# Performance work log

Measured on AMD Instinct MI355X. Metric: run time of the kernel, lower is better.

Reference implementation:

```python
import jax, jax.numpy as jnp
import numpy as np

N, E, H, NH, RBF = 20000, 200000, 128, 8, 64
HD = H // NH
CUT_HI = 5.0


def _ln(t, s, b, eps=1e-6):
    mu = t.mean(-1, keepdims=True)
    var = ((t - mu) ** 2).mean(-1, keepdims=True)
    return (t - mu) * jax.lax.rsqrt(var + eps) * s + b


def _cutoff(w):
    # cosine cutoff, cutoff_lower = 0
    return 0.5 * (jnp.cos(w * (jnp.pi / CUT_HI)) + 1.0) * (w < CUT_HI)


def _xavier(k, fi, fo):
    lim = float(np.sqrt(6.0 / (fi + fo)))
    return jax.random.uniform(k, (fi, fo), minval=-lim, maxval=lim, dtype=jnp.float32)


def setup_inputs() -> dict:
    key = jax.random.key(0)
    ks = jax.random.split(key, 16)
    return {
        "x": jax.random.normal(ks[0], (N, H), jnp.float32),
        "vec": jax.random.normal(ks[1], (N, 3, H), jnp.float32),
        "edge_weight": jax.random.uniform(ks[2], (E, 1), jnp.float32) * 6.0,
        "edge_attr": jax.random.uniform(ks[3], (E, RBF), jnp.float32),
        "edge_vec": jax.random.normal(ks[4], (E, 3), jnp.float32),
        "senders": jax.random.randint(ks[5], (E,), 0, N, jnp.int32),
        "receivers": jax.random.randint(ks[6], (E,), 0, N, jnp.int32),
        "ln_s": jnp.ones((H,), jnp.float32), "ln_b": jnp.zeros((H,), jnp.float32),
        "Wq": _xavier(ks[7], H, H), "bq": jnp.zeros((H,), jnp.float32),
        "Wk": _xavier(ks[8], H, H), "bk": jnp.zeros((H,), jnp.float32),
        "Wv": _xavier(ks[9], H, 3 * H), "bv": jnp.zeros((3 * H,), jnp.float32),
        "Wvec": _xavier(ks[10], H, 3 * H),
        "Wdk": _xavier(ks[11], RBF, H), "bdk": jnp.zeros((H,), jnp.float32),
        "Wdv": _xavier(ks[12], RBF, 3 * H), "bdv": jnp.zeros((3 * H,), jnp.float32),
        "Wo": _xavier(ks[13], H, 3 * H), "bo": jnp.zeros((3 * H,), jnp.float32),
        "qln_s": jnp.ones((HD,), jnp.float32), "qln_b": jnp.zeros((HD,), jnp.float32),
        "kln_s": jnp.ones((HD,), jnp.float32), "kln_b": jnp.zeros((HD,), jnp.float32),
    }


def reference(x, vec, edge_weight, edge_attr, edge_vec, senders, receivers,
              ln_s, ln_b, Wq, bq, Wk, bk, Wv, bv, Wvec, Wdk, bdk, Wdv, bdv,
              Wo, bo, qln_s, qln_b, kln_s, kln_b):
    act = jax.nn.silu
    n = x.shape[0]
    xn = _ln(x, ln_s, ln_b)                                    # [N,H]
    q = _ln((xn @ Wq + bq).reshape(n, NH, HD), qln_s, qln_b)   # [N,h,d]
    k = _ln((xn @ Wk + bk).reshape(n, NH, HD), kln_s, kln_b)   # [N,h,d]
    v = (xn @ Wv + bv).reshape(n, NH, 3 * HD)                  # [N,h,3d]
    vp = vec @ Wvec                                            # [N,3,3H]
    vec1, vec2, vec3 = jnp.split(vp, 3, axis=-1)               # [N,3,H] each
    vec_dot = (vec1 * vec2).sum(axis=1)                        # [N,H]
    vec_h = vec.reshape(n, 3, NH, HD)                          # [N,3,h,d]
    dk = act(edge_attr @ Wdk + bdk).reshape(-1, NH, HD)        # [E,h,d]
    dv = act(edge_attr @ Wdv + bdv).reshape(-1, NH, 3 * HD)    # [E,h,3d]
    # message
    attn = (q[receivers] * k[senders] * dk).sum(axis=-1)       # [E,h]
    attn = act(attn) * _cutoff(edge_weight)                    # [E,h]
    v_j = v[senders] * dv                                      # [E,h,3d]
    xm, m1, m2 = jnp.split(v_j, 3, axis=2)                     # [E,h,d]
    xm = xm * attn[:, :, None]                                 # [E,h,d]
    vec_m = vec_h[senders] * m1[:, None] + m2[:, None] * edge_vec[:, :, None, None]  # [E,3,h,d]
    # aggregate
    x_agg = jax.ops.segment_sum(xm, receivers, num_segments=n).reshape(n, H)
    vec_agg = jax.ops.segment_sum(vec_m, receivers, num_segments=n).reshape(n, 3, H)
    o1, o2, o3 = jnp.split(x_agg @ Wo + bo, 3, axis=1)         # [N,H] each
    dvec = vec3 * o1[:, None] + vec_agg                        # [N,3,H]
    dx = vec_dot * o2 + o3                                     # [N,H]
    return (dx, dvec)
```

## Files before the change

kernel.cpp:

```cpp
#include <hip/hip_runtime.h>
#include <stdint.h>

#define NN 20000
#define NE 200000

typedef __attribute__((ext_vector_type(8))) short bf16x8;
typedef __attribute__((ext_vector_type(4))) float f32x4;

__device__ __forceinline__ float bf2f(uint32_t u) {
  union { uint32_t i; float f; } v; v.i = u << 16; return v.f;
}
__device__ __forceinline__ uint16_t f2bf(float f) {
  union { float f; uint32_t i; } v; v.f = f;
  return (uint16_t)((v.i + 0x7fffu + ((v.i >> 16) & 1u)) >> 16);
}
__device__ __forceinline__ uint32_t pk2(float lo, float hi) {
  return (uint32_t)f2bf(lo) | ((uint32_t)f2bf(hi) << 16);
}
__device__ __forceinline__ float siluf(float x) { return x / (1.f + __expf(-x)); }
__device__ __forceinline__ float prod2(uint32_t q2, uint32_t k2, uint32_t d2) {
  return bf2f(q2 & 0xffffu) * bf2f(k2 & 0xffffu) * bf2f(d2 & 0xffffu)
       + bf2f(q2 >> 16) * bf2f(k2 >> 16) * bf2f(d2 >> 16);
}

__global__ void k_prep(const float* __restrict__ Wq, const float* __restrict__ Wk,
                       const float* __restrict__ Wv, const float* __restrict__ Wvec,
                       const float* __restrict__ Wdk, const float* __restrict__ Wdv,
                       const float* __restrict__ Wo, const float* __restrict__ bq,
                       const float* __restrict__ bk, const float* __restrict__ bv,
                       const float* __restrict__ bdk, const float* __restrict__ bdv,
                       uint16_t* __restrict__ WTqkv, uint16_t* __restrict__ WTvec,
                       uint16_t* __restrict__ WTdkv2, uint16_t* __restrict__ WTo,
                       float* __restrict__ Bqkv, float* __restrict__ Bdkv2) {
  int idx = blockIdx.x * 256 + threadIdx.x;
  if (idx < 81920) {
    int j = idx;
    float v;
    if (j < 16384)      { int c = j >> 7, k = j & 127; v = Wq[k * 128 + c]; }
    else if (j < 32768) { j -= 16384; int c = j >> 7, k = j & 127; v = Wk[k * 128 + c]; }
    else                { j -= 32768; int c = j >> 7, k = j & 127; v = Wv[k * 384 + c]; }
    WTqkv[idx] = f2bf(v);
    return;
  }
  idx -= 81920;
  if (idx < 49152) {
    int c = idx >> 7, k = idx & 127;
    WTvec[idx] = f2bf(Wvec[k * 384 + c]);
    return;
  }
  idx -= 49152;
  if (idx < 32768) {
    int rr = idx >> 6, k = idx & 63;
    float v;
    if (rr < 128) v = Wdk[k * 128 + rr];
    else {
      int j = rr - 128, p = j >> 7, hd = j & 127;
      int c = (hd >> 4) * 48 + p * 16 + (hd & 15);
      v = Wdv[k * 384 + c];
    }
    WTdkv2[idx] = f2bf(v);
    return;
  }
  idx -= 32768;
  if (idx < 49152) {
    int c = idx >> 7, k = idx & 127;
    WTo[idx] = f2bf(Wo[k * 384 + c]);
    return;
  }
  idx -= 49152;
  if (idx < 640) Bqkv[idx] = (idx < 128) ? bq[idx] : ((idx < 256) ? bk[idx - 128] : bv[idx - 256]);
  else if (idx < 1152) {
    int t = idx - 640;
    if (t < 128) Bdkv2[t] = bdk[t];
    else {
      int j = t - 128, p = j >> 7, hd = j & 127;
      Bdkv2[t] = bdv[(hd >> 4) * 48 + p * 16 + (hd & 15)];
    }
  }
}

__global__ void k_node_pre(const float* __restrict__ x, const float* __restrict__ s,
                           const float* __restrict__ b, const float* __restrict__ vec,
                           uint16_t* __restrict__ xn_b, uint16_t* __restrict__ vec_b) {
  if (blockIdx.x < 5000) {
    int gt = blockIdx.x * 256 + threadIdx.x;
    int node = gt >> 6, lane = gt & 63;
    if (node >= NN) return;
    const float* row = x + (size_t)node * 128;
    float2 v = *(const float2*)&row[lane * 2];
    float sum = v.x + v.y, sq = v.x * v.x + v.y * v.y;
    #pragma unroll
    for (int off = 32; off; off >>= 1) { sum += __shfl_xor(sum, off); sq += __shfl_xor(sq, off); }
    float mu = sum * (1.f / 128.f);
    float var = sq * (1.f / 128.f) - mu * mu;
    float rs = rsqrtf(var + 1e-6f);
    float o0 = (v.x - mu) * rs * s[lane * 2] + b[lane * 2];
    float o1 = (v.y - mu) * rs * s[lane * 2 + 1] + b[lane * 2 + 1];
    ((uint32_t*)xn_b)[(size_t)node * 64 + lane] = pk2(o0, o1);
  } else {
    int i = (blockIdx.x - 5000) * 256 + threadIdx.x;
    if (i >= NN * 3 * 64) return;
    float2 v = ((const float2*)vec)[i];
    ((uint32_t*)vec_b)[i] = pk2(v.x, v.y);
  }
}

__global__ void k_cast_bf16(const float* __restrict__ src, uint16_t* __restrict__ dst, int npairs) {
  int i = blockIdx.x * 256 + threadIdx.x;
  if (i >= npairs) return;
  float2 v = ((const float2*)src)[i];
  ((uint32_t*)dst)[i] = pk2(v.x, v.y);
}

__global__ void k_hist(const int* __restrict__ rcv, int* __restrict__ deg) {
  int e = blockIdx.x * 256 + threadIdx.x;
  if (e < NE) atomicAdd(&deg[rcv[e]], 1);
}

__global__ void k_scan1(const int* __restrict__ deg, int* __restrict__ bsum) {
  __shared__ int ws[4];
  int i = blockIdx.x * 256 + threadIdx.x;
  int x = (i < NN) ? deg[i] : 0;
  #pragma unroll
  for (int d = 32; d; d >>= 1) x += __shfl_xor(x, d);
  if ((threadIdx.x & 63) == 0) ws[threadIdx.x >> 6] = x;
  __syncthreads();
  if (threadIdx.x == 0) bsum[blockIdx.x] = ws[0] + ws[1] + ws[2] + ws[3];
}

__global__ void k_scan2(int* __restrict__ bsum, int nb, int* __restrict__ off) {
  int lane = threadIdx.x;
  int carry = 0;
  for (int base = 0; base < nb; base += 64) {
    int i = base + lane;
    int x = (i < nb) ? bsum[i] : 0;
    int v = x;
    #pragma unroll
    for (int d = 1; d < 64; d <<= 1) { int y = __shfl_up(v, d); if (lane >= d) v += y; }
    if (i < nb) bsum[i] = carry + v - x;
    carry += __shfl(v, 63);
  }
  if (lane == 0) off[NN] = carry;
}

__global__ void k_scan3(const int* __restrict__ deg, const int* __restrict__ bsum,
                        int* __restrict__ off, int* __restrict__ cur) {
  __shared__ int ws[4];
  int t = threadIdx.x, lane = t & 63, w = t >> 6;
  int i = blockIdx.x * 256 + t;
  int x = (i < NN) ? deg[i] : 0;
  int v = x;
  #pragma unroll
  for (int d = 1; d < 64; d <<= 1) { int y = __shfl_up(v, d); if (lane >= d) v += y; }
  if (lane == 63) ws[w] = v;
  __syncthreads();
  int wadd = 0;
  for (int j = 0; j < w; j++) wadd += ws[j];
  int excl = bsum[blockIdx.x] + wadd + v - x;
  if (i < NN) { off[i] = excl; cur[i] = excl; }
}

__global__ void k_scatter(const int* __restrict__ rcv, int* __restrict__ cur,
                          int* __restrict__ perm) {
  int e = blockIdx.x * 256 + threadIdx.x;
  if (e >= NE) return;
  int pos = atomicAdd(&cur[rcv[e]], 1);
  perm[pos] = e;
}

__global__ void k_permute(const float* __restrict__ ea, const int* __restrict__ perm,
                          const int* __restrict__ snd, const int* __restrict__ rcv,
                          const float* __restrict__ ew, const float* __restrict__ evec,
                          uint16_t* __restrict__ ea_perm, int* __restrict__ sndp,
                          int* __restrict__ rcvp, float4* __restrict__ edata) {
  int idx = blockIdx.x * 256 + threadIdx.x;
  if (idx >= NE * 16) return;
  int i = idx >> 4, j = idx & 15;
  int e = perm[i];
  float4 v = *(const float4*)&ea[(size_t)e * 64 + j * 4];
  uint2 o;
  o.x = pk2(v.x, v.y);
  o.y = pk2(v.z, v.w);
  *(uint2*)&ea_perm[(size_t)i * 64 + j * 4] = o;
  if (j == 0) {
    sndp[i] = snd[e];
    rcvp[i] = rcv[e];
    float w = ew[e];
    float cut = (w < 5.f) ? 0.5f * (__cosf(w * 0.628318530717958648f) + 1.f) : 0.f;
    edata[i] = make_float4(evec[e * 3], evec[e * 3 + 1], evec[e * 3 + 2], cut);
  }
}

template <int KTOT, bool OUT_BF16, bool SILU>
__global__ __launch_bounds__(256) void k_gemm(const uint16_t* __restrict__ A,
                                              const uint16_t* __restrict__ BT,
                                              const float* __restrict__ bias,
                                              void* __restrict__ Cout, int M, int Fo) {
  __shared__ __align__(16) uint16_t As[128 * 72];
  __shared__ __align__(16) uint16_t Bs[128 * 72];
  int t = threadIdx.x;
  int l = t & 63;
  int row0 = blockIdx.y * 128, col0 = blockIdx.x * 128;
  int wm = ((t >> 6) >> 1) * 64, wn = ((t >> 6) & 1) * 64;
  f32x4 acc[4][4] = {};
  for (int kt = 0; kt < KTOT; kt += 64) {
    __syncthreads();
    #pragma unroll
    for (int i = 0; i < 4; i++) {
      int c = i * 256 + t;
      int row = c >> 3, ko = (c & 7) * 8;
      uint4 av = make_uint4(0u, 0u, 0u, 0u);
      int gr = row0 + row;
      if (gr < M) av = *(const uint4*)&A[(size_t)gr * KTOT + kt + ko];
      *(uint4*)&As[row * 72 + ko] = av;
      uint4 bw = *(const uint4*)&BT[(size_t)(col0 + row) * KTOT + kt + ko];
      *(uint4*)&Bs[row * 72 + ko] = bw;
    }
    __syncthreads();
    #pragma unroll
    for (int kk = 0; kk < 64; kk += 32) {
      bf16x8 af[4], bfr[4];
      #pragma unroll
      for (int mf = 0; mf < 4; mf++)
        af[mf] = *(const bf16x8*)&As[(wm + mf * 16 + (l & 15)) * 72 + (l >> 4) * 8 + kk];
      #pragma unroll
      for (int nf = 0; nf < 4; nf++)
        bfr[nf] = *(const bf16x8*)&Bs[(wn + nf * 16 + (l & 15)) * 72 + (l >> 4) * 8 + kk];
      #pragma unroll
      for (int mf = 0; mf < 4; mf++)
        #pragma unroll
        for (int nf = 0; nf < 4; nf++)
          acc[mf][nf] = __builtin_amdgcn_mfma_f32_16x16x32_bf16(af[mf], bfr[nf], acc[mf][nf], 0, 0, 0);
    }
  }
  float* Cf = (float*)Cout;
  uint16_t* Cb = (uint16_t*)Cout;
  #pragma unroll
  for (int mf = 0; mf < 4; mf++) {
    #pragma unroll
    for (int r = 0; r < 4; r++) {
      int grow = row0 + wm + mf * 16 + (l >> 4) * 4 + r;
      if (grow >= M) continue;
      #pragma unroll
      for (int nf = 0; nf < 4; nf++) {
        int gcol = col0 + wn + nf * 16 + (l & 15);
        float v = acc[mf][nf][r];
        if (bias) v += bias[gcol];
        if (SILU) v = siluf(v);
        if (OUT_BF16) Cb[(size_t)grow * Fo + gcol] = f2bf(v);
        else          Cf[(size_t)grow * Fo + gcol] = v;
      }
    }
  }
}

__global__ void k_headln(const uint16_t* __restrict__ qkv, const float* __restrict__ qs,
                         const float* __restrict__ qb, const float* __restrict__ ks,
                         const float* __restrict__ kb, uint16_t* __restrict__ out) {
  int idx = blockIdx.x * 256 + threadIdx.x;
  if (idx >= NN * 16) return;
  int n = idx >> 4, ph = idx & 15, part = ph >> 3, h = ph & 7;
  const uint16_t* src = qkv + (size_t)n * 640 + part * 128 + h * 16;
  float v[16], sum = 0.f;
  #pragma unroll
  for (int i = 0; i < 16; i++) { v[i] = bf2f(src[i]); sum += v[i]; }
  float mu = sum * (1.f / 16.f), var = 0.f;
  #pragma unroll
  for (int i = 0; i < 16; i++) { float dd = v[i] - mu; var += dd * dd; }
  float rs = rsqrtf(var * (1.f / 16.f) + 1e-6f);
  const float* sc = part ? ks : qs;
  const float* bb = part ? kb : qb;
  uint16_t* dst = out + (size_t)n * 256 + part * 128 + h * 16;
  #pragma unroll
  for (int i = 0; i < 16; i++) dst[i] = f2bf((v[i] - mu) * rs * sc[i] + bb[i]);
}

__device__ __forceinline__ void mfma32(const uint16_t* As, int r0,
                                       const uint16_t* __restrict__ BT2, int cb,
                                       int wn, int l, f32x4 acc[2][2]) {
  #pragma unroll
  for (int kk = 0; kk < 2; kk++) {
    bf16x8 af[2];
    #pragma unroll
    for (int mf = 0; mf < 2; mf++)
      af[mf] = *(const bf16x8*)&As[(r0 + mf * 16 + (l & 15)) * 68 + (l >> 4) * 8 + kk * 32];
    #pragma unroll
    for (int nf = 0; nf < 2; nf++) {
      bf16x8 bv = *(const bf16x8*)&BT2[(size_t)(cb * 128 + wn + nf * 16 + (l & 15)) * 64 +
                                       (l >> 4) * 8 + kk * 32];
      #pragma unroll
      for (int mf = 0; mf < 2; mf++)
        acc[mf][nf] = __builtin_amdgcn_mfma_f32_16x16x32_bf16(af[mf], bv, acc[mf][nf], 0, 0, 0);
    }
  }
}

__device__ __forceinline__ void silu_store32(uint16_t* mt, const float* bsv,
                                             int wn, int l, f32x4 acc[2][2]) {
  #pragma unroll
  for (int mf = 0; mf < 2; mf++)
    #pragma unroll
    for (int r = 0; r < 4; r++) {
      int row = mf * 16 + (l >> 4) * 4 + r;
      #pragma unroll
      for (int nf = 0; nf < 2; nf++) {
        int c = wn + nf * 16 + (l & 15);
        mt[row * 140 + c] = f2bf(siluf(acc[mf][nf][r] + bsv[nf]));
      }
    }
}

__global__ __launch_bounds__(256) void k_edge_all(
    const uint16_t* __restrict__ eap, const int* __restrict__ sndp,
    const int* __restrict__ rcvp, const int* __restrict__ off,
    const float4* __restrict__ edata, const uint16_t* __restrict__ WT2,
    const float* __restrict__ Bd2, const uint16_t* __restrict__ qk_b,
    const uint16_t* __restrict__ qkv_b, const uint16_t* __restrict__ vec_b,
    float* __restrict__ xagg, float* __restrict__ vecagg) {
  __shared__ __align__(16) uint16_t As[64 * 68];
  __shared__ __align__(16) uint16_t mtA[32 * 140];
  __shared__ __align__(16) uint16_t mtB[32 * 140];
  __shared__ float attn_l[32 * 8];
  __shared__ int sndl[64], rcvl[64], lo_g[64], hi_g[64];
  __shared__ float4 ed4[64];

  int e0 = blockIdx.x * 64;
  int t = threadIdx.x, l = t & 63, wn = (t >> 6) * 32;

  if (t < 64) {
    int e = e0 + t;
    int r = rcvp[e];
    sndl[t] = sndp[e]; rcvl[t] = r;
    lo_g[t] = off[r]; hi_g[t] = off[r + 1];
    ed4[t] = edata[e];
  }
  #pragma unroll
  for (int i = 0; i < 2; i++) {
    int c = i * 256 + t;
    int row = c >> 3, ko = (c & 7) * 8;
    *(uint4*)&As[row * 68 + ko] = *(const uint4*)&eap[(size_t)(e0 + row) * 64 + ko];
  }
  float bs[4][2];
  #pragma unroll
  for (int cb = 0; cb < 4; cb++) {
    bs[cb][0] = Bd2[cb * 128 + wn + (l & 15)];
    bs[cb][1] = Bd2[cb * 128 + wn + 16 + (l & 15)];
  }
  __syncthreads();

  #pragma unroll
  for (int half = 0; half < 2; half++) {
    int r0 = half * 32;
    { f32x4 acc[2][2] = {}; mfma32(As, r0, WT2, 0, wn, l, acc); silu_store32(mtA, bs[0], wn, l, acc); }
    __syncthreads();
    {
      int el = t >> 3, h = t & 7;
      int ge = r0 + el;
      int rn = rcvl[ge], sn = sndl[ge];
      const uint32_t* qp = (const uint32_t*)(qk_b + (size_t)rn * 256 + h * 16);
      const uint32_t* kp = (const uint32_t*)(qk_b + (size_t)sn * 256 + 128 + h * 16);
      const uint32_t* dp = (const uint32_t*)&mtA[el * 140 + h * 16];
      float dot = 0.f;
      #pragma unroll
      for (int j = 0; j < 8; j++) dot += prod2(qp[j], kp[j], dp[j]);
      attn_l[el * 8 + h] = siluf(dot) * ed4[ge].w;
    }
    __syncthreads();
    { f32x4 acc[2][2] = {}; mfma32(As, r0, WT2, 1, wn, l, acc); silu_store32(mtA, bs[1], wn, l, acc); }
    __syncthreads();
    {
      int col = t & 127, sub = t >> 7;
      int i0 = r0 + sub * 16, i1 = i0 + 16;
      int voff = 256 + (col >> 4) * 48 + (col & 15);
      float accx = 0.f;
      #pragma unroll 8
      for (int i = i0; i < i1; i++) {
        int n = rcvl[i];
        float m = bf2f(mtA[(i - r0) * 140 + col]);
        float a = attn_l[(i - r0) * 8 + (col >> 4)];
        float v0 = bf2f(qkv_b[(size_t)sndl[i] * 640 + voff]);
        accx += v0 * m * a;
        if (i == i1 - 1 || rcvl[i + 1] != n) {
          float* dst = &xagg[(size_t)n * 128 + col];
          if (lo_g[i] >= e0 + i0 && hi_g[i] <= e0 + i1) *dst = accx;
          else atomicAdd(dst, accx);
          accx = 0.f;
        }
      }
    }
    __syncthreads();
    { f32x4 acc[2][2] = {}; mfma32(As, r0, WT2, 2, wn, l, acc); silu_store32(mtA, bs[2], wn, l, acc); }
    { f32x4 acc[2][2] = {}; mfma32(As, r0, WT2, 3, wn, l, acc); silu_store32(mtB, bs[3], wn, l, acc); }
    __syncthreads();
    {
      int col = t & 127, sub = t >> 7;
      int i0 = r0 + sub * 16, i1 = i0 + 16;
      int v1o = 256 + (col >> 4) * 48 + 16 + (col & 15);
      float a0 = 0.f, a1 = 0.f, a2 = 0.f;
      #pragma unroll 8
      for (int i = i0; i < i1; i++) {
        int n = rcvl[i];
        int s = sndl[i];
        float m1d = bf2f(mtA[(i - r0) * 140 + col]);
        float m2d = bf2f(mtB[(i - r0) * 140 + col]);
        const uint16_t* vb = qkv_b + (size_t)s * 640 + v1o;
        float mm1 = bf2f(vb[0]) * m1d;
        float mm2 = bf2f(vb[16]) * m2d;
        const uint16_t* vv = vec_b + (size_t)s * 384 + col;
        float4 ev = ed4[i];
        a0 += bf2f(vv[0])   * mm1 + ev.x * mm2;
        a1 += bf2f(vv[128]) * mm1 + ev.y * mm2;
        a2 += bf2f(vv[256]) * mm1 + ev.z * mm2;
        if (i == i1 - 1 || rcvl[i + 1] != n) {
          float* d0 = &vecagg[((size_t)n * 3 + 0) * 128 + col];
          float* d1 = &vecagg[((size_t)n * 3 + 1) * 128 + col];
          float* d2 = &vecagg[((size_t)n * 3 + 2) * 128 + col];
          if (lo_g[i] >= e0 + i0 && hi_g[i] <= e0 + i1) { *d0 = a0; *d1 = a1; *d2 = a2; }
          else { atomicAdd(d0, a0); atomicAdd(d1, a1); atomicAdd(d2, a2); }
          a0 = a1 = a2 = 0.f;
        }
      }
    }
    __syncthreads();
  }
}

__global__ void k_final(const float* __restrict__ o, const uint16_t* __restrict__ vp,
                        float* __restrict__ dx, float* __restrict__ dvec) {
  int idx = blockIdx.x * 256 + threadIdx.x;
  if (idx >= NN * 128) return;
  int n = idx >> 7, j = idx & 127;
  const float* op = o + (size_t)n * 384;
  float o1 = op[j], o2 = op[128 + j], o3 = op[256 + j];
  const uint16_t* vpn = vp + (size_t)n * 3 * 384;
  float vd = 0.f;
  #pragma unroll
  for (int c = 0; c < 3; c++)
    vd += bf2f(vpn[c * 384 + j]) * bf2f(vpn[c * 384 + 128 + j]);
  dx[idx] = vd * o2 + o3;
  #pragma unroll
  for (int c = 0; c < 3; c++) {
    size_t vi = ((size_t)n * 3 + c) * 128 + j;
    dvec[vi] = bf2f(vpn[c * 384 + 256 + j]) * o1 + dvec[vi];
  }
}

static inline int cdiv_i(long long a, long long b) { return (int)((a + b - 1) / b); }

extern "C" void kernel_launch(void* const* d_in, const int* in_sizes, int n_in,
                              void* d_out, int out_size, void* d_ws, size_t ws_size,
                              hipStream_t stream) {
  const float* x    = (const float*)d_in[0];
  const float* vec  = (const float*)d_in[1];
  const float* ew   = (const float*)d_in[2];
  const float* ea   = (const float*)d_in[3];
  const float* evec = (const float*)d_in[4];
  const int*   snd  = (const int*)d_in[5];
  const int*   rcv  = (const int*)d_in[6];
  const float* ln_s = (const float*)d_in[7];
  const float* ln_b = (const float*)d_in[8];
  const float* Wq = (const float*)d_in[9];   const float* bq = (const float*)d_in[10];
  const float* Wk = (const float*)d_in[11];  const float* bk = (const float*)d_in[12];
  const float* Wv = (const float*)d_in[13];  const float* bv = (const float*)d_in[14];
  const float* Wvec = (const float*)d_in[15];
  const float* Wdk = (const float*)d_in[16]; const float* bdk = (const float*)d_in[17];
  const float* Wdv = (const float*)d_in[18]; const float* bdv = (const float*)d_in[19];
  const float* Wo = (const float*)d_in[20];  const float* bo = (const float*)d_in[21];
  const float* qln_s = (const float*)d_in[22]; const float* qln_b = (const float*)d_in[23];
  const float* kln_s = (const float*)d_in[24]; const float* kln_b = (const float*)d_in[25];
  (void)in_sizes; (void)n_in; (void)ws_size;

  uint8_t* p = (uint8_t*)d_ws;
  auto alloc = [&](size_t bytes) -> uint8_t* {
    uint8_t* r = p; p += (bytes + 255) & ~(size_t)255; return r;
  };
  uint16_t* WTqkv = (uint16_t*)alloc(640 * 128 * 2);
  float*    Bqkv  = (float*)alloc(640 * 4);
  uint16_t* WTvec = (uint16_t*)alloc(384 * 128 * 2);
  uint16_t* WTdkv = (uint16_t*)alloc(512 * 64 * 2);
  float*    Bdkv  = (float*)alloc(512 * 4);
  uint16_t* WTo   = (uint16_t*)alloc(384 * 128 * 2);
  int*      deg   = (int*)alloc(NN * 4);
  int*      off   = (int*)alloc((NN + 1) * 4);
  int*      cur   = (int*)alloc(NN * 4);
  int*      bsum  = (int*)alloc(256 * 4);
  int*      perm  = (int*)alloc((size_t)NE * 4);
  int*      sndp  = (int*)alloc((size_t)NE * 4);
  int*      rcvp  = (int*)alloc((size_t)NE * 4);
  float4*   edata = (float4*)alloc((size_t)NE * 16);
  uint16_t* ea_perm = (uint16_t*)alloc((size_t)NE * 64 * 2);
  uint16_t* xn_b  = (uint16_t*)alloc((size_t)NN * 128 * 2);
  uint16_t* qkv_b = (uint16_t*)alloc((size_t)NN * 640 * 2);
  uint16_t* qk_b  = (uint16_t*)alloc((size_t)NN * 256 * 2);
  uint16_t* vec_b = (uint16_t*)alloc((size_t)NN * 3 * 128 * 2);
  uint16_t* vp    = (uint16_t*)alloc((size_t)NN * 3 * 384 * 2);
  float*    o      = (float*)alloc((size_t)NN * 384 * 4);
  uint16_t* xagg_b = (uint16_t*)alloc((size_t)NN * 128 * 2);

  float* xagg   = (float*)d_out;
  float* vecagg = (float*)d_out + (size_t)NN * 128;

  hipMemsetAsync(d_out, 0, (size_t)out_size * 4, stream);

  k_prep<<<cdiv_i(81920 + 49152 + 32768 + 49152 + 1152, 256), 256, 0, stream>>>(
      Wq, Wk, Wv, Wvec, Wdk, Wdv, Wo, bq, bk, bv, bdk, bdv,
      WTqkv, WTvec, WTdkv, WTo, Bqkv, Bdkv);

  int NSB = cdiv_i(NN, 256);
  hipMemsetAsync(deg, 0, NN * 4, stream);
  k_hist<<<cdiv_i(NE, 256), 256, 0, stream>>>(rcv, deg);
  k_scan1<<<NSB, 256, 0, stream>>>(deg, bsum);
  k_scan2<<<1, 64, 0, stream>>>(bsum, NSB, off);
  k_scan3<<<NSB, 256, 0, stream>>>(deg, bsum, off, cur);
  k_scatter<<<cdiv_i(NE, 256), 256, 0, stream>>>(rcv, cur, perm);
  k_permute<<<cdiv_i((long long)NE * 16, 256), 256, 0, stream>>>(ea, perm, snd, rcv, ew, evec,
                                                                 ea_perm, sndp, rcvp, edata);

  k_node_pre<<<5000 + cdiv_i((long long)NN * 3 * 64, 256), 256, 0, stream>>>(
      x, ln_s, ln_b, vec, xn_b, vec_b);

  { dim3 g(640 / 128, cdiv_i(NN, 128));
    k_gemm<128, true, false><<<g, 256, 0, stream>>>(xn_b, WTqkv, Bqkv, qkv_b, NN, 640); }
  k_headln<<<cdiv_i((long long)NN * 16, 256), 256, 0, stream>>>(qkv_b, qln_s, qln_b, kln_s, kln_b, qk_b);

  { dim3 g(384 / 128, cdiv_i((long long)NN * 3, 128));
    k_gemm<128, true, false><<<g, 256, 0, stream>>>(vec_b, WTvec, nullptr, vp, NN * 3, 384); }

  k_edge_all<<<NE / 64, 256, 0, stream>>>(ea_perm, sndp, rcvp, off, edata, WTdkv, Bdkv,
                                          qk_b, qkv_b, vec_b, xagg, vecagg);

  k_cast_bf16<<<cdiv_i((long long)NN * 64, 256), 256, 0, stream>>>(xagg, xagg_b, NN * 64);
  { dim3 g(384 / 128, cdiv_i(NN, 128));
    k_gemm<128, false, false><<<g, 256, 0, stream>>>(xagg_b, WTo, bo, o, NN, 384); }

  k_final<<<cdiv_i((long long)NN * 128, 256), 256, 0, stream>>>(o, vp, xagg, vecagg);
}
```

Baseline: 361.9 us.

## Interleave v and vec per channel and fuse edge message passes

```diff
diff --git a/kernel.cpp b/kernel.cpp
--- a/kernel.cpp
+++ b/kernel.cpp
@@ -18,10 +18,6 @@
   return (uint32_t)f2bf(lo) | ((uint32_t)f2bf(hi) << 16);
 }
 __device__ __forceinline__ float siluf(float x) { return x / (1.f + __expf(-x)); }
-__device__ __forceinline__ float prod2(uint32_t q2, uint32_t k2, uint32_t d2) {
-  return bf2f(q2 & 0xffffu) * bf2f(k2 & 0xffffu) * bf2f(d2 & 0xffffu)
-       + bf2f(q2 >> 16) * bf2f(k2 >> 16) * bf2f(d2 >> 16);
-}
 
 __global__ void k_prep(const float* __restrict__ Wq, const float* __restrict__ Wk,
                        const float* __restrict__ Wv, const float* __restrict__ Wvec,
@@ -33,16 +29,19 @@
                        uint16_t* __restrict__ WTdkv2, uint16_t* __restrict__ WTo,
                        float* __restrict__ Bqkv, float* __restrict__ Bdkv2) {
   int idx = blockIdx.x * 256 + threadIdx.x;
-  if (idx < 81920) {
-    int j = idx;
+  if (idx < 98304) {
+    int rr = idx >> 7, k = idx & 127;
     float v;
-    if (j < 16384)      { int c = j >> 7, k = j & 127; v = Wq[k * 128 + c]; }
-    else if (j < 32768) { j -= 16384; int c = j >> 7, k = j & 127; v = Wk[k * 128 + c]; }
-    else                { j -= 32768; int c = j >> 7, k = j & 127; v = Wv[k * 384 + c]; }
+    if (rr < 128)      v = Wq[k * 128 + rr];
+    else if (rr < 256) v = Wk[k * 128 + rr - 128];
+    else {
+      int j2 = rr - 256, j = j2 >> 2, c = j2 & 3;
+      v = (c < 3) ? Wv[k * 384 + (j >> 4) * 48 + c * 16 + (j & 15)] : 0.f;
+    }
     WTqkv[idx] = f2bf(v);
     return;
   }
-  idx -= 81920;
+  idx -= 98304;
   if (idx < 49152) {
     int c = idx >> 7, k = idx & 127;
     WTvec[idx] = f2bf(Wvec[k * 384 + c]);
@@ -55,8 +54,7 @@
     if (rr < 128) v = Wdk[k * 128 + rr];
     else {
       int j = rr - 128, p = j >> 7, hd = j & 127;
-      int c = (hd >> 4) * 48 + p * 16 + (hd & 15);
-      v = Wdv[k * 384 + c];
+      v = Wdv[k * 384 + (hd >> 4) * 48 + p * 16 + (hd & 15)];
     }
     WTdkv2[idx] = f2bf(v);
     return;
@@ -68,9 +66,15 @@
     return;
   }
   idx -= 49152;
-  if (idx < 640) Bqkv[idx] = (idx < 128) ? bq[idx] : ((idx < 256) ? bk[idx - 128] : bv[idx - 256]);
-  else if (idx < 1152) {
-    int t = idx - 640;
+  if (idx < 768) {
+    if (idx < 128)      Bqkv[idx] = bq[idx];
+    else if (idx < 256) Bqkv[idx] = bk[idx - 128];
+    else {
+      int j2 = idx - 256, j = j2 >> 2, c = j2 & 3;
+      Bqkv[idx] = (c < 3) ? bv[(j >> 4) * 48 + c * 16 + (j & 15)] : 0.f;
+    }
+  } else if (idx < 1280) {
+    int t = idx - 768;
     if (t < 128) Bdkv2[t] = bdk[t];
     else {
       int j = t - 128, p = j >> 7, hd = j & 127;
@@ -81,7 +85,8 @@
 
 __global__ void k_node_pre(const float* __restrict__ x, const float* __restrict__ s,
                            const float* __restrict__ b, const float* __restrict__ vec,
-                           uint16_t* __restrict__ xn_b, uint16_t* __restrict__ vec_b) {
+                           uint16_t* __restrict__ xn_b, uint16_t* __restrict__ vec_b,
+                           uint16_t* __restrict__ vec_w) {
   if (blockIdx.x < 5000) {
     int gt = blockIdx.x * 256 + threadIdx.x;
     int node = gt >> 6, lane = gt & 63;
@@ -97,11 +102,18 @@
     float o0 = (v.x - mu) * rs * s[lane * 2] + b[lane * 2];
     float o1 = (v.y - mu) * rs * s[lane * 2 + 1] + b[lane * 2 + 1];
     ((uint32_t*)xn_b)[(size_t)node * 64 + lane] = pk2(o0, o1);
-  } else {
+  } else if (blockIdx.x < 20000) {
     int i = (blockIdx.x - 5000) * 256 + threadIdx.x;
-    if (i >= NN * 3 * 64) return;
     float2 v = ((const float2*)vec)[i];
     ((uint32_t*)vec_b)[i] = pk2(v.x, v.y);
+  } else {
+    int i = (blockIdx.x - 20000) * 256 + threadIdx.x;
+    int n = i >> 7, j = i & 127;
+    const float* vr = vec + (size_t)n * 384 + j;
+    uint2 o;
+    o.x = pk2(vr[0], vr[128]);
+    o.y = pk2(vr[256], 0.f);
+    *(uint2*)&vec_w[(size_t)n * 512 + j * 4] = o;
   }
 }
 
@@ -260,7 +272,7 @@
   int idx = blockIdx.x * 256 + threadIdx.x;
   if (idx >= NN * 16) return;
   int n = idx >> 4, ph = idx & 15, part = ph >> 3, h = ph & 7;
-  const uint16_t* src = qkv + (size_t)n * 640 + part * 128 + h * 16;
+  const uint16_t* src = qkv + (size_t)n * 768 + part * 128 + h * 16;
   float v[16], sum = 0.f;
   #pragma unroll
   for (int i = 0; i < 16; i++) { v[i] = bf2f(src[i]); sum += v[i]; }
@@ -275,6 +287,8 @@
   for (int i = 0; i < 16; i++) dst[i] = f2bf((v[i] - mu) * rs * sc[i] + bb[i]);
 }
 
+#define MTS 516
+
 __device__ __forceinline__ void mfma32(const uint16_t* As, int r0,
                                        const uint16_t* __restrict__ BT2, int cb,
                                        int wn, int l, f32x4 acc[2][2]) {
@@ -295,8 +309,8 @@
   }
 }
 
-__device__ __forceinline__ void silu_store32(uint16_t* mt, const float* bsv,
-                                             int wn, int l, f32x4 acc[2][2]) {
+__device__ __forceinline__ void silu_slot(uint16_t* mt, const float bsv[2], int slot,
+                                          int wn, int l, f32x4 acc[2][2]) {
   #pragma unroll
   for (int mf = 0; mf < 2; mf++)
     #pragma unroll
@@ -305,7 +319,7 @@
       #pragma unroll
       for (int nf = 0; nf < 2; nf++) {
         int c = wn + nf * 16 + (l & 15);
-        mt[row * 140 + c] = f2bf(siluf(acc[mf][nf][r] + bsv[nf]));
+        mt[row * MTS + c * 4 + slot] = f2bf(siluf(acc[mf][nf][r] + bsv[nf]));
       }
     }
 }
@@ -315,11 +329,10 @@
     const int* __restrict__ rcvp, const int* __restrict__ off,
     const float4* __restrict__ edata, const uint16_t* __restrict__ WT2,
     const float* __restrict__ Bd2, const uint16_t* __restrict__ qk_b,
-    const uint16_t* __restrict__ qkv_b, const uint16_t* __restrict__ vec_b,
+    const uint16_t* __restrict__ qkv_b, const uint16_t* __restrict__ vec_w,
     float* __restrict__ xagg, float* __restrict__ vecagg) {
   __shared__ __align__(16) uint16_t As[64 * 68];
-  __shared__ __align__(16) uint16_t mtA[32 * 140];
-  __shared__ __align__(16) uint16_t mtB[32 * 140];
+  __shared__ __align__(16) uint16_t mt[32 * MTS];
   __shared__ float attn_l[32 * 8];
   __shared__ int sndl[64], rcvl[64], lo_g[64], hi_g[64];
   __shared__ float4 ed4[64];
@@ -351,73 +364,63 @@
   #pragma unroll
   for (int half = 0; half < 2; half++) {
     int r0 = half * 32;
-    { f32x4 acc[2][2] = {}; mfma32(As, r0, WT2, 0, wn, l, acc); silu_store32(mtA, bs[0], wn, l, acc); }
+    { f32x4 acc[2][2] = {}; mfma32(As, r0, WT2, 0, wn, l, acc); silu_slot(mt, bs[0], 3, wn, l, acc); }
     __syncthreads();
     {
       int el = t >> 3, h = t & 7;
       int ge = r0 + el;
       int rn = rcvl[ge], sn = sndl[ge];
-      const uint32_t* qp = (const uint32_t*)(qk_b + (size_t)rn * 256 + h * 16);
-      const uint32_t* kp = (const uint32_t*)(qk_b + (size_t)sn * 256 + 128 + h * 16);
-      const uint32_t* dp = (const uint32_t*)&mtA[el * 140 + h * 16];
+      const uint16_t* qb_ = qk_b + (size_t)rn * 256 + h * 16;
+      const uint16_t* kb_ = qk_b + (size_t)sn * 256 + 128 + h * 16;
+      uint4 q0 = *(const uint4*)qb_;
+      uint4 q1 = *(const uint4*)(qb_ + 8);
+      uint4 k0 = *(const uint4*)kb_;
+      uint4 k1 = *(const uint4*)(kb_ + 8);
+      { f32x4 acc[2][2] = {}; mfma32(As, r0, WT2, 1, wn, l, acc); silu_slot(mt, bs[1], 0, wn, l, acc); }
+      { f32x4 acc[2][2] = {}; mfma32(As, r0, WT2, 2, wn, l, acc); silu_slot(mt, bs[2], 1, wn, l, acc); }
+      { f32x4 acc[2][2] = {}; mfma32(As, r0, WT2, 3, wn, l, acc); silu_slot(mt, bs[3], 2, wn, l, acc); }
+      const uint16_t* dkr = &mt[el * MTS + h * 64 + 3];
+      uint32_t qa[8] = {q0.x, q0.y, q0.z, q0.w, q1.x, q1.y, q1.z, q1.w};
+      uint32_t ka[8] = {k0.x, k0.y, k0.z, k0.w, k1.x, k1.y, k1.z, k1.w};
       float dot = 0.f;
       #pragma unroll
-      for (int j = 0; j < 8; j++) dot += prod2(qp[j], kp[j], dp[j]);
+      for (int j = 0; j < 8; j++) {
+        dot += bf2f(qa[j] & 0xffffu) * bf2f(ka[j] & 0xffffu) * bf2f(dkr[j * 8]);
+        dot += bf2f(qa[j] >> 16)     * bf2f(ka[j] >> 16)     * bf2f(dkr[j * 8 + 4]);
+      }
       attn_l[el * 8 + h] = siluf(dot) * ed4[ge].w;
     }
-    __syncthreads();
-    { f32x4 acc[2][2] = {}; mfma32(As, r0, WT2, 1, wn, l, acc); silu_store32(mtA, bs[1], wn, l, acc); }
     __syncthreads();
     {
       int col = t & 127, sub = t >> 7;
       int i0 = r0 + sub * 16, i1 = i0 + 16;
-      int voff = 256 + (col >> 4) * 48 + (col & 15);
-      float accx = 0.f;
+      int ha = col >> 4;
+      float accx = 0.f, a0 = 0.f, a1 = 0.f, a2 = 0.f;
       #pragma unroll 8
       for (int i = i0; i < i1; i++) {
-        int n = rcvl[i];
-        float m = bf2f(mtA[(i - r0) * 140 + col]);
-        float a = attn_l[(i - r0) * 8 + (col >> 4)];
-        float v0 = bf2f(qkv_b[(size_t)sndl[i] * 640 + voff]);
-        accx += v0 * m * a;
+        int li = i - r0;
+        int n = rcvl[i], s = sndl[i];
+        uint2 vt = *(const uint2*)&qkv_b[(size_t)s * 768 + 256 + col * 4];
+        uint2 wt = *(const uint2*)&vec_w[(size_t)s * 512 + col * 4];
+        uint2 mr = *(const uint2*)&mt[li * MTS + col * 4];
+        float a = attn_l[li * 8 + ha];
+        float xmv = bf2f(mr.x & 0xffffu), m1v = bf2f(mr.x >> 16), m2v = bf2f(mr.y & 0xffffu);
+        accx += bf2f(vt.x & 0xffffu) * xmv * a;
+        float mm1 = bf2f(vt.x >> 16) * m1v;
+        float mm2 = bf2f(vt.y & 0xffffu) * m2v;
+        float4 ev = ed4[i];
+        a0 += bf2f(wt.x & 0xffffu) * mm1 + ev.x * mm2;
+        a1 += bf2f(wt.x >> 16)     * mm1 + ev.y * mm2;
+        a2 += bf2f(wt.y & 0xffffu) * mm1 + ev.z * mm2;
         if (i == i1 - 1 || rcvl[i + 1] != n) {
-          float* dst = &xagg[(size_t)n * 128 + col];
-          if (lo_g[i] >= e0 + i0 && hi_g[i] <= e0 + i1) *dst = accx;
-          else atomicAdd(dst, accx);
-          accx = 0.f;
-        }
-      }
-    }
-    __syncthreads();
-    { f32x4 acc[2][2] = {}; mfma32(As, r0, WT2, 2, wn, l, acc); silu_store32(mtA, bs[2], wn, l, acc); }
-    { f32x4 acc[2][2] = {}; mfma32(As, r0, WT2, 3, wn, l, acc); silu_store32(mtB, bs[3], wn, l, acc); }
-    __syncthreads();
-    {
-      int col = t & 127, sub = t >> 7;
-      int i0 = r0 + sub * 16, i1 = i0 + 16;
-      int v1o = 256 + (col >> 4) * 48 + 16 + (col & 15);
-      float a0 = 0.f, a1 = 0.f, a2 = 0.f;
-      #pragma unroll 8
-      for (int i = i0; i < i1; i++) {
-        int n = rcvl[i];
-        int s = sndl[i];
-        float m1d = bf2f(mtA[(i - r0) * 140 + col]);
-        float m2d = bf2f(mtB[(i - r0) * 140 + col]);
-        const uint16_t* vb = qkv_b + (size_t)s * 640 + v1o;
-        float mm1 = bf2f(vb[0]) * m1d;
-        float mm2 = bf2f(vb[16]) * m2d;
-        const uint16_t* vv = vec_b + (size_t)s * 384 + col;
-        float4 ev = ed4[i];
-        a0 += bf2f(vv[0])   * mm1 + ev.x * mm2;
-        a1 += bf2f(vv[128]) * mm1 + ev.y * mm2;
-        a2 += bf2f(vv[256]) * mm1 + ev.z * mm2;
-        if (i == i1 - 1 || rcvl[i + 1] != n) {
+          bool cont = (lo_g[i] >= e0 + i0) && (hi_g[i] <= e0 + i1);
+          float* dx_ = &xagg[(size_t)n * 128 + col];
           float* d0 = &vecagg[((size_t)n * 3 + 0) * 128 + col];
           float* d1 = &vecagg[((size_t)n * 3 + 1) * 128 + col];
           float* d2 = &vecagg[((size_t)n * 3 + 2) * 128 + col];
-          if (lo_g[i] >= e0 + i0 && hi_g[i] <= e0 + i1) { *d0 = a0; *d1 = a1; *d2 = a2; }
-          else { atomicAdd(d0, a0); atomicAdd(d1, a1); atomicAdd(d2, a2); }
-          a0 = a1 = a2 = 0.f;
+          if (cont) { *dx_ = accx; *d0 = a0; *d1 = a1; *d2 = a2; }
+          else { atomicAdd(dx_, accx); atomicAdd(d0, a0); atomicAdd(d1, a1); atomicAdd(d2, a2); }
+          accx = a0 = a1 = a2 = 0.f;
         }
       }
     }
@@ -474,8 +477,8 @@
   auto alloc = [&](size_t bytes) -> uint8_t* {
     uint8_t* r = p; p += (bytes + 255) & ~(size_t)255; return r;
   };
-  uint16_t* WTqkv = (uint16_t*)alloc(640 * 128 * 2);
-  float*    Bqkv  = (float*)alloc(640 * 4);
+  uint16_t* WTqkv = (uint16_t*)alloc(768 * 128 * 2);
+  float*    Bqkv  = (float*)alloc(768 * 4);
   uint16_t* WTvec = (uint16_t*)alloc(384 * 128 * 2);
   uint16_t* WTdkv = (uint16_t*)alloc(512 * 64 * 2);
   float*    Bdkv  = (float*)alloc(512 * 4);
@@ -490,9 +493,10 @@
   float4*   edata = (float4*)alloc((size_t)NE * 16);
   uint16_t* ea_perm = (uint16_t*)alloc((size_t)NE * 64 * 2);
   uint16_t* xn_b  = (uint16_t*)alloc((size_t)NN * 128 * 2);
-  uint16_t* qkv_b = (uint16_t*)alloc((size_t)NN * 640 * 2);
+  uint16_t* qkv_b = (uint16_t*)alloc((size_t)NN * 768 * 2);
   uint16_t* qk_b  = (uint16_t*)alloc((size_t)NN * 256 * 2);
   uint16_t* vec_b = (uint16_t*)alloc((size_t)NN * 3 * 128 * 2);
+  uint16_t* vec_w = (uint16_t*)alloc((size_t)NN * 512 * 2);
   uint16_t* vp    = (uint16_t*)alloc((size_t)NN * 3 * 384 * 2);
   float*    o      = (float*)alloc((size_t)NN * 384 * 4);
   uint16_t* xagg_b = (uint16_t*)alloc((size_t)NN * 128 * 2);
@@ -502,7 +506,7 @@
 
   hipMemsetAsync(d_out, 0, (size_t)out_size * 4, stream);
 
-  k_prep<<<cdiv_i(81920 + 49152 + 32768 + 49152 + 1152, 256), 256, 0, stream>>>(
+  k_prep<<<cdiv_i(98304 + 49152 + 32768 + 49152 + 1280, 256), 256, 0, stream>>>(
       Wq, Wk, Wv, Wvec, Wdk, Wdv, Wo, bq, bk, bv, bdk, bdv,
       WTqkv, WTvec, WTdkv, WTo, Bqkv, Bdkv);
 
@@ -516,18 +520,17 @@
   k_permute<<<cdiv_i((long long)NE * 16, 256), 256, 0, stream>>>(ea, perm, snd, rcv, ew, evec,
                                                                  ea_perm, sndp, rcvp, edata);
 
-  k_node_pre<<<5000 + cdiv_i((long long)NN * 3 * 64, 256), 256, 0, stream>>>(
-      x, ln_s, ln_b, vec, xn_b, vec_b);
-
-  { dim3 g(640 / 128, cdiv_i(NN, 128));
-    k_gemm<128, true, false><<<g, 256, 0, stream>>>(xn_b, WTqkv, Bqkv, qkv_b, NN, 640); }
+  k_node_pre<<<30000, 256, 0, stream>>>(x, ln_s, ln_b, vec, xn_b, vec_b, vec_w);
+
+  { dim3 g(768 / 128, cdiv_i(NN, 128));
+    k_gemm<128, true, false><<<g, 256, 0, stream>>>(xn_b, WTqkv, Bqkv, qkv_b, NN, 768); }
   k_headln<<<cdiv_i((long long)NN * 16, 256), 256, 0, stream>>>(qkv_b, qln_s, qln_b, kln_s, kln_b, qk_b);
 
   { dim3 g(384 / 128, cdiv_i((long long)NN * 3, 128));
     k_gemm<128, true, false><<<g, 256, 0, stream>>>(vec_b, WTvec, nullptr, vp, NN * 3, 384); }
 
   k_edge_all<<<NE / 64, 256, 0, stream>>>(ea_perm, sndp, rcvp, off, edata, WTdkv, Bdkv,
-                                          qk_b, qkv_b, vec_b, xagg, vecagg);
+                                          qk_b, qkv_b, vec_w, xagg, vecagg);
 
   k_cast_bf16<<<cdiv_i((long long)NN * 64, 256), 256, 0, stream>>>(xagg, xagg_b, NN * 64);
   { dim3 g(384 / 128, cdiv_i(NN, 128));
```

Measured after the change: 347.9 us. 1.04x faster.
